# Optimization experiments

Measured on AMD Instinct MI355X. Metric: run time of the kernel, lower is better.

The kernel has to match this reference:

```python
import jax, jax.numpy as jnp
import numpy as np

B, S, H = 2, 2048, 1024
E, K = 16, 2
CF = 1.5
IMP_THRESH = 0.5
CAP_MAX = int(B * S * CF * K / E)  # 768, capacity when adaptive_k == K


def setup_inputs() -> dict:
    key = jax.random.key(0)
    ks = jax.random.split(key, 8)
    def xavier(k, shape):
        fan_in, fan_out = shape[0], shape[1]
        std = np.sqrt(2.0 / (fan_in + fan_out))
        return jax.random.normal(k, shape, dtype=jnp.float32) * std
    return {
        'hidden_states': jax.random.normal(ks[0], (B, S, H), dtype=jnp.float32),
        # router: Linear(H,H) -> ReLU -> Linear(H,E)
        'W1': xavier(ks[1], (H, H)), 'b1': jnp.zeros((H,), jnp.float32),
        'W2': xavier(ks[2], (H, E)), 'b2': jnp.zeros((E,), jnp.float32),
        # importance predictor: Linear(H,H//2) -> ReLU -> Linear(H//2,1) -> Sigmoid
        'Wi1': xavier(ks[3], (H, H // 2)), 'bi1': jnp.zeros((H // 2,), jnp.float32),
        'Wi2': xavier(ks[4], (H // 2, 1)), 'bi2': jnp.zeros((1,), jnp.float32),
        # top_k predictor: Linear(H+1,H//4) -> ReLU -> Linear(H//4,K) -> Softmax
        'Wt1': xavier(ks[5], (H + 1, H // 4)), 'bt1': jnp.zeros((H // 4,), jnp.float32),
        'Wt2': xavier(ks[6], (H // 4, K)), 'bt2': jnp.zeros((K,), jnp.float32),
    }


def reference(hidden_states, W1, b1, W2, b2, Wi1, bi1, Wi2, bi2, Wt1, bt1, Wt2, bt2):
    # importance scores [B,S]
    imp_h = jax.nn.relu(hidden_states @ Wi1 + bi1)
    importance = jax.nn.sigmoid(jnp.squeeze(imp_h @ Wi2 + bi2, -1))

    # adaptive top-k (traced scalar in [1, K])
    avg_feat = hidden_states.mean((0, 1))                       # [H]
    combined = jnp.concatenate([avg_feat, importance.mean()[None]])  # [H+1]
    tk_probs = jax.nn.softmax(jax.nn.relu(combined @ Wt1 + bt1) @ Wt2 + bt2)
    adaptive_k = jnp.minimum(jnp.argmax(tk_probs) + 1, K).astype(jnp.int32)

    # router logits -> probs -> top-k
    logits = jax.nn.relu(hidden_states @ W1 + b1) @ W2 + b2     # [B,S,E]
    router_probs = jax.nn.softmax(logits, axis=-1)
    topk_p, topk_i = jax.lax.top_k(router_probs, K)             # [B,S,K], sorted desc

    # only the first adaptive_k slots are active (== torch.topk with k=adaptive_k)
    slot_valid = (jnp.arange(K) < adaptive_k)                   # [K] bool
    p = topk_p * slot_valid.astype(topk_p.dtype)
    p = p / (p.sum(-1, keepdims=True) + 1e-8)

    # capacity-limited dispatch/combine (vectorized version of the b,s,k loop)
    cap_eff = jnp.floor(jnp.float32(B * S) * CF * adaptive_k.astype(jnp.float32) / E).astype(jnp.int32)
    N = B * S * K
    e_flat = topk_i.reshape(N)                                  # expert id per (b,s,k) in loop order
    p_flat = p.reshape(N)
    valid = jnp.broadcast_to(slot_valid, (B * S, K)).reshape(N)
    oh = jax.nn.one_hot(e_flat, E, dtype=jnp.float32) * valid[:, None].astype(jnp.float32)  # [N,E]
    # position within expert = running count of earlier valid assignments to same expert
    pos = (jnp.cumsum(oh, axis=0)[jnp.arange(N), e_flat] - 1.0).astype(jnp.int32)
    write = valid & (pos >= 0) & (pos < cap_eff)
    pos_c = jnp.clip(pos, 0, CAP_MAX - 1)
    t_idx = jnp.arange(N) // K                                  # flat token index
    wf = write.astype(p_flat.dtype)
    dispatch = jnp.zeros((B * S, E, CAP_MAX), p.dtype).at[t_idx, e_flat, pos_c].add(wf)
    combine = jnp.zeros((B * S, E, CAP_MAX), p.dtype).at[t_idx, e_flat, pos_c].add(wf * p_flat)
    dispatch = dispatch.reshape(B, S, E, CAP_MAX)
    combine = combine.reshape(B, S, E, CAP_MAX)

    # load-balancing aux loss
    prob_per_expert = router_probs.mean((0, 1))                 # [E]
    usage = oh.sum(0) / (jnp.float32(B * S) * adaptive_k.astype(jnp.float32))
    aux_loss = jnp.sum(prob_per_expert * usage) * E

    # importance re-weighting of combine tensor
    iw = (importance > IMP_THRESH).astype(combine.dtype)
    combine = combine * (1.0 + iw[:, :, None, None])

    return dispatch, combine, router_probs, aux_loss, importance
```

## Files before the change

### kernel.cpp

```cpp
#include <hip/hip_runtime.h>
#include <math.h>

#define TOK   4096
#define HD    1024
#define NEXP  16
#define CAPM  768

static const size_t DISP_OFF = 0;
static const size_t COMB_OFF = 50331648;
static const size_t RP_OFF   = 100663296;
static const size_t AUX_OFF  = 100728832;
static const size_t IMP_OFF  = 100728833;

#define WS_IMPZ   0
#define WS_COLSUM 4096
#define WS_T1PRE  5120
#define WS_PROBS  5376
#define WS_AK     5392
#define WS_TOPKP  5400
#define WS_TOPKI  13592
#define WS_ZEROF  5400

__global__ __launch_bounds__(256) void kA(
    const float* __restrict__ x, const float* __restrict__ W1,
    const float* __restrict__ b1, const float* __restrict__ Wi1,
    const float* __restrict__ bi1, const float* __restrict__ Wi2,
    float* __restrict__ h1out, float* __restrict__ impz)
{
    __shared__ __align__(16) float As[16][68];
    __shared__ __align__(16) float Bs[16][128];
    __shared__ float red[64];

    const int tid = threadIdx.x;
    const int tx = tid & 15;
    const int ty = tid >> 4;
    const int n0 = blockIdx.x * 128;
    const int m0 = blockIdx.y * 64;
    const bool isW1 = (n0 < HD);
    const float* __restrict__ Bp = isW1 ? (W1 + n0) : (Wi1 + (n0 - HD));
    const int ldb = isW1 ? 1024 : 512;

    const int am = tid >> 2, akq = tid & 3;
    const int br = tid >> 5, bq = tid & 31;

    if (tid < 64) red[tid] = 0.f;

    float acc[4][8];
#pragma unroll
    for (int i = 0; i < 4; ++i)
#pragma unroll
        for (int j = 0; j < 8; ++j) acc[i][j] = 0.f;

#pragma unroll 1
    for (int kt = 0; kt < 64; ++kt) {
        const float4 av  = *(const float4*)(x + (size_t)(m0 + am) * HD + kt * 16 + akq * 4);
        const float4 bv0 = *(const float4*)(Bp + (size_t)(kt * 16 + br) * ldb + bq * 4);
        const float4 bv1 = *(const float4*)(Bp + (size_t)(kt * 16 + 8 + br) * ldb + bq * 4);
        __syncthreads();
        As[akq * 4 + 0][am] = av.x;
        As[akq * 4 + 1][am] = av.y;
        As[akq * 4 + 2][am] = av.z;
        As[akq * 4 + 3][am] = av.w;
        *(float4*)&Bs[br][bq * 4]     = bv0;
        *(float4*)&Bs[8 + br][bq * 4] = bv1;
        __syncthreads();
#pragma unroll 4
        for (int kk = 0; kk < 16; ++kk) {
            const float4 a   = *(const float4*)&As[kk][ty * 4];
            const float4 b0  = *(const float4*)&Bs[kk][tx * 4];
            const float4 b1v = *(const float4*)&Bs[kk][tx * 4 + 64];
            const float avv[4] = { a.x, a.y, a.z, a.w };
            const float bvv[8] = { b0.x, b0.y, b0.z, b0.w, b1v.x, b1v.y, b1v.z, b1v.w };
#pragma unroll
            for (int i = 0; i < 4; ++i)
#pragma unroll
                for (int j = 0; j < 8; ++j)
                    acc[i][j] = fmaf(avv[i], bvv[j], acc[i][j]);
        }
    }

    if (isW1) {
        const float4 bb0 = *(const float4*)(b1 + n0 + tx * 4);
        const float4 bb1 = *(const float4*)(b1 + n0 + tx * 4 + 64);
        const float bvv[8] = { bb0.x, bb0.y, bb0.z, bb0.w, bb1.x, bb1.y, bb1.z, bb1.w };
#pragma unroll
        for (int i = 0; i < 4; ++i) {
            const int m = m0 + ty * 4 + i;
            float4 o0, o1;
            o0.x = fmaxf(acc[i][0] + bvv[0], 0.f);
            o0.y = fmaxf(acc[i][1] + bvv[1], 0.f);
            o0.z = fmaxf(acc[i][2] + bvv[2], 0.f);
            o0.w = fmaxf(acc[i][3] + bvv[3], 0.f);
            o1.x = fmaxf(acc[i][4] + bvv[4], 0.f);
            o1.y = fmaxf(acc[i][5] + bvv[5], 0.f);
            o1.z = fmaxf(acc[i][6] + bvv[6], 0.f);
            o1.w = fmaxf(acc[i][7] + bvv[7], 0.f);
            *(float4*)(h1out + (size_t)m * HD + n0 + tx * 4)      = o0;
            *(float4*)(h1out + (size_t)m * HD + n0 + tx * 4 + 64) = o1;
        }
    } else {
        const int nW = n0 - HD;
        const float4 bb0 = *(const float4*)(bi1 + nW + tx * 4);
        const float4 bb1 = *(const float4*)(bi1 + nW + tx * 4 + 64);
        const float4 w0  = *(const float4*)(Wi2 + nW + tx * 4);
        const float4 w1  = *(const float4*)(Wi2 + nW + tx * 4 + 64);
        const float bvv[8] = { bb0.x, bb0.y, bb0.z, bb0.w, bb1.x, bb1.y, bb1.z, bb1.w };
        const float wvv[8] = { w0.x, w0.y, w0.z, w0.w, w1.x, w1.y, w1.z, w1.w };
        __syncthreads();
#pragma unroll
        for (int i = 0; i < 4; ++i) {
            float s = 0.f;
#pragma unroll
            for (int j = 0; j < 8; ++j)
                s += fmaxf(acc[i][j] + bvv[j], 0.f) * wvv[j];
            atomicAdd(&red[ty * 4 + i], s);
        }
        __syncthreads();
        if (tid < 64) atomicAdd(&impz[m0 + tid], red[tid]);
    }
}

__global__ void kSig(const float* __restrict__ impz, const float* __restrict__ bi2,
                     float* __restrict__ impOut)
{
    const int t = blockIdx.x * 256 + threadIdx.x;
    const float z = impz[t] + bi2[0];
    impOut[t] = 1.f / (1.f + expf(-z));
}

__global__ void kAvg(const float* __restrict__ x, float* __restrict__ colsum)
{
    const int c = blockIdx.x * 256 + threadIdx.x;
    const int r0 = blockIdx.y * 64;
    float s = 0.f;
    for (int r = r0; r < r0 + 64; ++r) s += x[(size_t)r * HD + c];
    atomicAdd(&colsum[c], s);
}

__global__ void kTk1(const float* __restrict__ colsum, const float* __restrict__ Wt1,
                     float* __restrict__ t1pre)
{
    const int j = threadIdx.x;
    const int i0 = blockIdx.x * 32;
    float s = 0.f;
    for (int i = i0; i < i0 + 32; ++i)
        s = fmaf(colsum[i] * (1.f / TOK), Wt1[i * 256 + j], s);
    atomicAdd(&t1pre[j], s);
}

__global__ void kTk2(const float* __restrict__ imp, const float* __restrict__ t1pre,
                     const float* __restrict__ Wt1, const float* __restrict__ bt1,
                     const float* __restrict__ Wt2, const float* __restrict__ bt2,
                     int* __restrict__ akOut)
{
    __shared__ float sm[256];
    const int tid = threadIdx.x;
    float s = 0.f;
    for (int i = 0; i < 16; ++i) s += imp[tid + i * 256];
    sm[tid] = s;
    __syncthreads();
    for (int off = 128; off > 0; off >>= 1) {
        if (tid < off) sm[tid] += sm[tid + off];
        __syncthreads();
    }
    const float imp_mean = sm[0] * (1.f / TOK);
    __syncthreads();
    const float t1 = fmaxf(t1pre[tid] + imp_mean * Wt1[1024 * 256 + tid] + bt1[tid], 0.f);
    sm[tid] = t1 * Wt2[tid * 2 + 0];
    __syncthreads();
    for (int off = 128; off > 0; off >>= 1) {
        if (tid < off) sm[tid] += sm[tid + off];
        __syncthreads();
    }
    const float l0 = sm[0] + bt2[0];
    __syncthreads();
    sm[tid] = t1 * Wt2[tid * 2 + 1];
    __syncthreads();
    for (int off = 128; off > 0; off >>= 1) {
        if (tid < off) sm[tid] += sm[tid + off];
        __syncthreads();
    }
    const float l1 = sm[0] + bt2[1];
    if (tid == 0) akOut[0] = (l1 > l0) ? 2 : 1;
}

__global__ __launch_bounds__(256) void kLog(
    const float* __restrict__ h1, const float* __restrict__ W2,
    const float* __restrict__ b2, float* __restrict__ rp,
    float* __restrict__ topkP, int* __restrict__ topkI,
    float* __restrict__ probsum)
{
    __shared__ float lg[16][17];
    __shared__ float ex[16][17];
    __shared__ float ps[16];
    const int tid = threadIdx.x;
    const int e  = tid & 15;
    const int tt = tid >> 4;
    const int t  = blockIdx.x * 16 + tt;
    const float* __restrict__ hrow = h1 + (size_t)t * HD;
    float s0 = 0.f, s1 = 0.f, s2 = 0.f, s3 = 0.f;
#pragma unroll 4
    for (int k = 0; k < HD; k += 4) {
        const float4 h = *(const float4*)(hrow + k);
        s0 = fmaf(h.x, W2[(k + 0) * NEXP + e], s0);
        s1 = fmaf(h.y, W2[(k + 1) * NEXP + e], s1);
        s2 = fmaf(h.z, W2[(k + 2) * NEXP + e], s2);
        s3 = fmaf(h.w, W2[(k + 3) * NEXP + e], s3);
    }
    const float logit = (s0 + s1) + (s2 + s3) + b2[e];
    lg[tt][e] = logit;
    if (tid < 16) ps[tid] = 0.f;
    __syncthreads();
    float mx = -1e30f;
#pragma unroll
    for (int j = 0; j < 16; ++j) mx = fmaxf(mx, lg[tt][j]);
    const float my_ex = expf(logit - mx);
    ex[tt][e] = my_ex;
    __syncthreads();
    float sum = 0.f;
#pragma unroll
    for (int j = 0; j < 16; ++j) sum += ex[tt][j];
    const float p = my_ex / sum;
    rp[(size_t)t * NEXP + e] = p;
    lg[tt][e] = p;
    atomicAdd(&ps[e], p);
    __syncthreads();
    if (e == 0) {
        float pv[16];
#pragma unroll
        for (int j = 0; j < 16; ++j) pv[j] = lg[tt][j];
        int i0 = 0; float v0 = pv[0];
#pragma unroll
        for (int j = 1; j < 16; ++j) if (pv[j] > v0) { v0 = pv[j]; i0 = j; }
        int i1 = -1; float v1 = -1e30f;
#pragma unroll
        for (int j = 0; j < 16; ++j) if (j != i0 && pv[j] > v1) { v1 = pv[j]; i1 = j; }
        topkP[t * 2] = v0; topkP[t * 2 + 1] = v1;
        topkI[t * 2] = i0; topkI[t * 2 + 1] = i1;
    }
    if (tid < 16) atomicAdd(&probsum[tid], ps[tid]);
}

__global__ __launch_bounds__(256) void kScan(
    const float* __restrict__ topkP, const int* __restrict__ topkI,
    const int* __restrict__ akPtr, const float* __restrict__ probsum,
    const float* __restrict__ imp, float* __restrict__ disp,
    float* __restrict__ comb, float* __restrict__ aux)
{
    __shared__ int cnt[256][16];
    __shared__ int totals[16];
    const int tid = threadIdx.x;
    const int ak = akPtr[0];
    const int cap = 384 * ak;
    int c[16];
#pragma unroll
    for (int e = 0; e < 16; ++e) c[e] = 0;
    const int n0 = tid * 32;
    for (int j = 0; j < 32; ++j) {
        const int n = n0 + j;
        if ((n & 1) < ak) c[topkI[n]]++;
    }
#pragma unroll
    for (int e = 0; e < 16; ++e) cnt[tid][e] = c[e];
    __syncthreads();
    if (tid < 16) {
        int run = 0;
        for (int i = 0; i < 256; ++i) { const int v = cnt[i][tid]; cnt[i][tid] = run; run += v; }
        totals[tid] = run;
    }
    __syncthreads();
#pragma unroll
    for (int e = 0; e < 16; ++e) c[e] = cnt[tid][e];
    for (int j = 0; j < 32; ++j) {
        const int n = n0 + j;
        const int k = n & 1;
        if (k < ak) {
            const int e = topkI[n];
            const int pos = c[e]++;
            if (pos < cap) {
                const int t = n >> 1;
                const float p0 = topkP[t * 2], p1 = topkP[t * 2 + 1];
                const float ssum = (ak == 2) ? (p0 + p1) : p0;
                const float pv = ((k == 0) ? p0 : p1) / (ssum + 1e-8f);
                const float iw = (imp[t] > 0.5f) ? 2.f : 1.f;
                const size_t idx = (size_t)t * (NEXP * CAPM) + (size_t)e * CAPM + pos;
                disp[idx] = 1.f;
                comb[idx] = pv * iw;
            }
        }
    }
    if (tid == 0) {
        float a = 0.f;
        const float invAk = 1.f / (float)(TOK * ak);
        for (int e = 0; e < 16; ++e)
            a += (probsum[e] * (1.f / TOK)) * ((float)totals[e] * invAk);
        aux[0] = a * (float)NEXP;
    }
}

extern "C" void kernel_launch(void* const* d_in, const int* in_sizes, int n_in,
                              void* d_out, int out_size, void* d_ws, size_t ws_size,
                              hipStream_t stream)
{
    const float* x   = (const float*)d_in[0];
    const float* W1  = (const float*)d_in[1];
    const float* b1  = (const float*)d_in[2];
    const float* W2  = (const float*)d_in[3];
    const float* b2  = (const float*)d_in[4];
    const float* Wi1 = (const float*)d_in[5];
    const float* bi1 = (const float*)d_in[6];
    const float* Wi2 = (const float*)d_in[7];
    const float* bi2 = (const float*)d_in[8];
    const float* Wt1 = (const float*)d_in[9];
    const float* bt1 = (const float*)d_in[10];
    const float* Wt2 = (const float*)d_in[11];
    const float* bt2 = (const float*)d_in[12];
    (void)in_sizes; (void)n_in; (void)out_size; (void)ws_size;

    float* out = (float*)d_out;
    float* wsF = (float*)d_ws;
    int*   akP = (int*)(wsF + WS_AK);

    hipMemsetAsync(d_ws, 0, (size_t)WS_ZEROF * 4, stream);

    float* h1scratch = out + DISP_OFF;

    kA  <<<dim3(12, 64), 256, 0, stream>>>(x, W1, b1, Wi1, bi1, Wi2,
                                           h1scratch, wsF + WS_IMPZ);
    kSig<<<16, 256, 0, stream>>>(wsF + WS_IMPZ, bi2, out + IMP_OFF);
    kAvg<<<dim3(4, 64), 256, 0, stream>>>(x, wsF + WS_COLSUM);
    kTk1<<<32, 256, 0, stream>>>(wsF + WS_COLSUM, Wt1, wsF + WS_T1PRE);
    kTk2<<<1, 256, 0, stream>>>(out + IMP_OFF, wsF + WS_T1PRE, Wt1, bt1, Wt2, bt2, akP);
    kLog<<<256, 256, 0, stream>>>(h1scratch, W2, b2, out + RP_OFF,
                                  wsF + WS_TOPKP, (int*)(wsF + WS_TOPKI), wsF + WS_PROBS);
    hipMemsetAsync(out, 0, (size_t)COMB_OFF * 2 * sizeof(float), stream);
    kScan<<<1, 256, 0, stream>>>(wsF + WS_TOPKP, (int*)(wsF + WS_TOPKI), akP,
                                 wsF + WS_PROBS, out + IMP_OFF,
                                 out + DISP_OFF, out + COMB_OFF, out + AUX_OFF);
}
```

Baseline: 656.6 us.

## Double-buffer kA GEMM tiles with K=32 and zero outputs via nontemporal kernel

The kA GEMM now uses a K-tile of 32 with two shared-memory buffers. Global loads for the next tile are issued into registers before the current tile's FMAs, which removes one of the two barriers per iteration and overlaps memory latency with compute. The launch-bounds hint asks for 3 blocks per SM, which may force register pressure or spills. Separately, the 400MB output memset is replaced by a custom kernel that writes zeros with nontemporal vector stores, which may be faster or slower than the runtime memset.

Measured after the change: 673.8 us. 1.03x slower.

```diff
diff --git a/kernel.cpp b/kernel.cpp
--- a/kernel.cpp
+++ b/kernel.cpp
@@ -21,14 +21,24 @@
 #define WS_TOPKI  13592
 #define WS_ZEROF  5400
 
-__global__ __launch_bounds__(256) void kA(
+typedef float v4f __attribute__((ext_vector_type(4)));
+
+__global__ __launch_bounds__(256) void kZero(v4f* __restrict__ p, int n4)
+{
+    const v4f z = (v4f)(0.f);
+    const int stride = gridDim.x * 256;
+    for (int i = blockIdx.x * 256 + threadIdx.x; i < n4; i += stride)
+        __builtin_nontemporal_store(z, p + i);
+}
+
+__global__ __launch_bounds__(256, 3) void kA(
     const float* __restrict__ x, const float* __restrict__ W1,
     const float* __restrict__ b1, const float* __restrict__ Wi1,
     const float* __restrict__ bi1, const float* __restrict__ Wi2,
     float* __restrict__ h1out, float* __restrict__ impz)
 {
-    __shared__ __align__(16) float As[16][68];
-    __shared__ __align__(16) float Bs[16][128];
+    __shared__ __align__(16) float As[2][32][68];
+    __shared__ __align__(16) float Bs[2][32][128];
     __shared__ float red[64];
 
     const int tid = threadIdx.x;
@@ -40,8 +50,10 @@
     const float* __restrict__ Bp = isW1 ? (W1 + n0) : (Wi1 + (n0 - HD));
     const int ldb = isW1 ? 1024 : 512;
 
-    const int am = tid >> 2, akq = tid & 3;
-    const int br = tid >> 5, bq = tid & 31;
+    const int am  = tid >> 3;
+    const int akq = tid & 7;
+    const int br = tid >> 5;
+    const int bq = tid & 31;
 
     if (tid < 64) red[tid] = 0.f;
 
@@ -51,31 +63,64 @@
 #pragma unroll
         for (int j = 0; j < 8; ++j) acc[i][j] = 0.f;
 
+    const float* pA0 = x + (size_t)(m0 + am) * HD + akq * 4;
+    const float* pA1 = x + (size_t)(m0 + 32 + am) * HD + akq * 4;
+    const float* pB  = Bp + (size_t)br * ldb + bq * 4;
+
+    float4 ra0 = *(const float4*)(pA0);
+    float4 ra1 = *(const float4*)(pA1);
+    float4 rb0 = *(const float4*)(pB);
+    float4 rb1 = *(const float4*)(pB + (size_t)8  * ldb);
+    float4 rb2 = *(const float4*)(pB + (size_t)16 * ldb);
+    float4 rb3 = *(const float4*)(pB + (size_t)24 * ldb);
+    {
+        As[0][akq * 4 + 0][am] = ra0.x; As[0][akq * 4 + 1][am] = ra0.y;
+        As[0][akq * 4 + 2][am] = ra0.z; As[0][akq * 4 + 3][am] = ra0.w;
+        As[0][akq * 4 + 0][am + 32] = ra1.x; As[0][akq * 4 + 1][am + 32] = ra1.y;
+        As[0][akq * 4 + 2][am + 32] = ra1.z; As[0][akq * 4 + 3][am + 32] = ra1.w;
+        *(float4*)&Bs[0][br][bq * 4]      = rb0;
+        *(float4*)&Bs[0][br + 8][bq * 4]  = rb1;
+        *(float4*)&Bs[0][br + 16][bq * 4] = rb2;
+        *(float4*)&Bs[0][br + 24][bq * 4] = rb3;
+    }
+    __syncthreads();
+
 #pragma unroll 1
-    for (int kt = 0; kt < 64; ++kt) {
-        const float4 av  = *(const float4*)(x + (size_t)(m0 + am) * HD + kt * 16 + akq * 4);
-        const float4 bv0 = *(const float4*)(Bp + (size_t)(kt * 16 + br) * ldb + bq * 4);
-        const float4 bv1 = *(const float4*)(Bp + (size_t)(kt * 16 + 8 + br) * ldb + bq * 4);
-        __syncthreads();
-        As[akq * 4 + 0][am] = av.x;
-        As[akq * 4 + 1][am] = av.y;
-        As[akq * 4 + 2][am] = av.z;
-        As[akq * 4 + 3][am] = av.w;
-        *(float4*)&Bs[br][bq * 4]     = bv0;
-        *(float4*)&Bs[8 + br][bq * 4] = bv1;
-        __syncthreads();
+    for (int kt = 0; kt < 32; ++kt) {
+        const int buf = kt & 1;
+        if (kt < 31) {
+            const int ko = (kt + 1) * 32;
+            ra0 = *(const float4*)(pA0 + ko);
+            ra1 = *(const float4*)(pA1 + ko);
+            rb0 = *(const float4*)(pB + (size_t)(ko +  0) * ldb);
+            rb1 = *(const float4*)(pB + (size_t)(ko +  8) * ldb);
+            rb2 = *(const float4*)(pB + (size_t)(ko + 16) * ldb);
+            rb3 = *(const float4*)(pB + (size_t)(ko + 24) * ldb);
+        }
 #pragma unroll 4
-        for (int kk = 0; kk < 16; ++kk) {
-            const float4 a   = *(const float4*)&As[kk][ty * 4];
-            const float4 b0  = *(const float4*)&Bs[kk][tx * 4];
-            const float4 b1v = *(const float4*)&Bs[kk][tx * 4 + 64];
+        for (int kk = 0; kk < 32; ++kk) {
+            const float4 a   = *(const float4*)&As[buf][kk][ty * 4];
+            const float4 f0  = *(const float4*)&Bs[buf][kk][tx * 4];
+            const float4 f1  = *(const float4*)&Bs[buf][kk][tx * 4 + 64];
             const float avv[4] = { a.x, a.y, a.z, a.w };
-            const float bvv[8] = { b0.x, b0.y, b0.z, b0.w, b1v.x, b1v.y, b1v.z, b1v.w };
+            const float bvv[8] = { f0.x, f0.y, f0.z, f0.w, f1.x, f1.y, f1.z, f1.w };
 #pragma unroll
             for (int i = 0; i < 4; ++i)
 #pragma unroll
                 for (int j = 0; j < 8; ++j)
                     acc[i][j] = fmaf(avv[i], bvv[j], acc[i][j]);
+        }
+        if (kt < 31) {
+            const int nb = buf ^ 1;
+            As[nb][akq * 4 + 0][am] = ra0.x; As[nb][akq * 4 + 1][am] = ra0.y;
+            As[nb][akq * 4 + 2][am] = ra0.z; As[nb][akq * 4 + 3][am] = ra0.w;
+            As[nb][akq * 4 + 0][am + 32] = ra1.x; As[nb][akq * 4 + 1][am + 32] = ra1.y;
+            As[nb][akq * 4 + 2][am + 32] = ra1.z; As[nb][akq * 4 + 3][am + 32] = ra1.w;
+            *(float4*)&Bs[nb][br][bq * 4]      = rb0;
+            *(float4*)&Bs[nb][br + 8][bq * 4]  = rb1;
+            *(float4*)&Bs[nb][br + 16][bq * 4] = rb2;
+            *(float4*)&Bs[nb][br + 24][bq * 4] = rb3;
+            __syncthreads();
         }
     }
 
@@ -321,7 +366,7 @@
     float* wsF = (float*)d_ws;
     int*   akP = (int*)(wsF + WS_AK);
 
-    hipMemsetAsync(d_ws, 0, (size_t)WS_ZEROF * 4, stream);
+    (void)hipMemsetAsync(d_ws, 0, (size_t)WS_ZEROF * 4, stream);
 
     float* h1scratch = out + DISP_OFF;
 
@@ -333,7 +378,7 @@
     kTk2<<<1, 256, 0, stream>>>(out + IMP_OFF, wsF + WS_T1PRE, Wt1, bt1, Wt2, bt2, akP);
     kLog<<<256, 256, 0, stream>>>(h1scratch, W2, b2, out + RP_OFF,
                                   wsF + WS_TOPKP, (int*)(wsF + WS_TOPKI), wsF + WS_PROBS);
-    hipMemsetAsync(out, 0, (size_t)COMB_OFF * 2 * sizeof(float), stream);
+    kZero<<<4096, 256, 0, stream>>>((v4f*)out, 25165824);
     kScan<<<1, 256, 0, stream>>>(wsF + WS_TOPKP, (int*)(wsF + WS_TOPKI), akP,
                                  wsF + WS_PROBS, out + IMP_OFF,
                                  out + DISP_OFF, out + COMB_OFF, out + AUX_OFF);
```
